# Optimization experiments

Measured on AMD Instinct MI355X. Metric: run time of the kernel, lower is better.

Reference implementation:

```python
import jax, jax.numpy as jnp
import numpy as np

PAD = 0

def setup_inputs() -> dict:
    key = jax.random.key(0)
    ks = jax.random.split(key, 16)
    B, S, D, F = 64, 512, 768, 256
    VOCAB = 32000
    # variable-length tweets: length in [8, S], rest is padding (token id PAD=0)
    lengths = jax.random.randint(ks[0], (B,), 8, S + 1)
    tok = jax.random.randint(ks[1], (B, S), 1, VOCAB)
    x = jnp.where(jnp.arange(S)[None, :] < lengths[:, None], tok, PAD)
    h = jax.random.normal(ks[2], (B, S, D), dtype=jnp.float32)
    sc = 0.02
    w2 = jax.random.normal(ks[3], (F, D, 2), dtype=jnp.float32) * sc
    b2 = jax.random.normal(ks[4], (F,), dtype=jnp.float32) * sc
    w3 = jax.random.normal(ks[5], (F, D, 3), dtype=jnp.float32) * sc
    b3 = jax.random.normal(ks[6], (F,), dtype=jnp.float32) * sc
    w4 = jax.random.normal(ks[7], (F, D, 4), dtype=jnp.float32) * sc
    b4 = jax.random.normal(ks[8], (F,), dtype=jnp.float32) * sc
    w5 = jax.random.normal(ks[9], (F, D, 5), dtype=jnp.float32) * sc
    b5 = jax.random.normal(ks[10], (F,), dtype=jnp.float32) * sc
    fc_w = jax.random.normal(ks[11], (1, 4 * F), dtype=jnp.float32) * sc
    fc_b = jax.random.normal(ks[12], (1,), dtype=jnp.float32) * sc
    return {"x": x, "h": h, "w2": w2, "b2": b2, "w3": w3, "b3": b3,
            "w4": w4, "b4": b4, "w5": w5, "b5": b5, "fc_w": fc_w, "fc_b": fc_b}


def _branch(hc, L, w, b):
    # hc: [B, D, S] front-compacted hidden states; w: [F, D, k]
    k = w.shape[-1]
    out = jax.lax.conv_general_dilated(
        hc, w, window_strides=(1,), padding='VALID',
        dimension_numbers=('NCH', 'OIH', 'NCH')) + b[None, :, None]  # [B,F,S-k+1]
    T = out.shape[-1]
    # conv position t is valid iff t + k - 1 < L  <=>  t < L - k + 1
    valid = jnp.arange(T)[None, :] < (L - k + 1)[:, None]           # [B,T]
    neg = jnp.asarray(-jnp.inf, out.dtype)
    pooled = jnp.max(jnp.where(valid[:, None, :], out, neg), axis=-1)  # [B,F]
    return jax.nn.relu(pooled)


def reference(x, h, w2, b2, w3, b3, w4, b4, w5, b5, fc_w, fc_b):
    mask = x != PAD                                   # [B,S]
    L = mask.sum(axis=1)                              # [B]
    # stable compaction: move non-pad token hidden states to the front, order preserved
    order = jnp.argsort(jnp.logical_not(mask), axis=1, stable=True)   # [B,S]
    hc = jnp.take_along_axis(h, order[..., None], axis=1)             # [B,S,D]
    hc = hc.transpose(0, 2, 1)                                        # [B,D,S]
    feats = jnp.concatenate([
        _branch(hc, L, w2, b2),
        _branch(hc, L, w3, b3),
        _branch(hc, L, w4, b4),
        _branch(hc, L, w5, b5),
    ], axis=-1)                                       # [B, 4F]
    logits = feats @ fc_w.T + fc_b                    # [B,1]
    return jax.nn.sigmoid(logits).squeeze(-1)         # [B]
```

## Files before the change

### kernel.cpp

```cpp
#include <hip/hip_runtime.h>
#include <stdint.h>

#define Bn 64
#define Sn 512
#define SPn 520
#define Dn 768
#define JSTRIDE 196608
#define ABUF 16640
#define BSLOT 8192
#define QS_A 28.222222f
#define SAQ 0.035433072f

typedef int iv4 __attribute__((ext_vector_type(4)));

static __device__ __forceinline__ signed char q8(float f, float s) {
  float t = __builtin_rintf(f * s);
  t = fmaxf(-127.f, fminf(127.f, t));
  return (signed char)(int)t;
}

static __device__ __forceinline__ void gload16(const void* g, void* l) {
  __builtin_amdgcn_global_load_lds(
      (const __attribute__((address_space(1))) unsigned int*)g,
      (__attribute__((address_space(3))) unsigned int*)l, 16, 0, 0);
}

template<int S, typename T, int N>
static __device__ __forceinline__ T (&sel(T (&a)[N], T (&b)[N]))[N] {
  if constexpr (S) return b; else return a;
}

__global__ __launch_bounds__(256) void stage_kernel(
    const int* __restrict__ x, const float* __restrict__ h,
    const float* __restrict__ w2, const float* __restrict__ w3,
    const float* __restrict__ w4, const float* __restrict__ w5,
    signed char* __restrict__ hcq, signed char* __restrict__ wq,
    float* __restrict__ fscale, int* __restrict__ Lout) {
  int tid = threadIdx.x, lane = tid & 63, wv = tid >> 6;
  if (blockIdx.x < 512) {
    int cidx = blockIdx.x;
    int b = cidx >> 3, rblk = cidx & 7;
    __shared__ unsigned long long masks[8];
    __shared__ short sidx[Sn];
    for (int c = wv; c < 8; c += 4) {
      unsigned long long m = __ballot(x[b * Sn + c * 64 + lane] != 0);
      if (lane == 0) masks[c] = m;
    }
    __syncthreads();
    int pref[9]; pref[0] = 0;
    #pragma unroll
    for (int c = 0; c < 8; ++c) pref[c + 1] = pref[c] + __popcll(masks[c]);
    int L = pref[8];
    if (rblk == 0 && tid == 0) Lout[b] = L;
    for (int p = tid; p < Sn; p += 256) {
      int c = p >> 6, l = p & 63;
      unsigned long long m = masks[c];
      if ((m >> l) & 1ull)
        sidx[pref[c] + __popcll(m & ((1ull << l) - 1ull))] = (short)p;
    }
    __syncthreads();
    int r0 = rblk * 65;
    for (int r = r0 + wv; r < r0 + 65; r += 4) {
      if (r < L) {
        signed char* dst = hcq + ((size_t)b * SPn + r) * Dn;
        const float* src = h + ((size_t)b * Sn + sidx[r]) * Dn;
        #pragma unroll
        for (int c = 0; c < 3; ++c) {
          int d = c * 256 + lane * 4;
          float4 v = *(const float4*)(src + d);
          char4 o = { q8(v.x, QS_A), q8(v.y, QS_A), q8(v.z, QS_A), q8(v.w, QS_A) };
          *(char4*)(dst + d) = o;
        }
      }
    }
  } else {
    __shared__ float sf[3840];
    __shared__ float smax[4];
    int bb = blockIdx.x - 512;
    int br = bb >> 8, f = bb & 255, k = br + 2;
    const float* w = (br == 0) ? w2 : (br == 1) ? w3 : (br == 2) ? w4 : w5;
    int mBase = 256 * ((br * (br + 3)) >> 1);
    const float* src = w + (size_t)f * Dn * k;
    int n = Dn * k;
    float mx = 0.f;
    for (int e = tid; e < n; e += 256) {
      float v = src[e];
      sf[e] = v;
      mx = fmaxf(mx, fabsf(v));
    }
    #pragma unroll
    for (int off = 32; off; off >>= 1) mx = fmaxf(mx, __shfl_xor(mx, off));
    if (lane == 0) smax[wv] = mx;
    __syncthreads();
    float M = fmaxf(fmaxf(smax[0], smax[1]), fmaxf(smax[2], smax[3]));
    M = fmaxf(M, 1e-30f);
    if (tid == 0) fscale[br * 256 + f] = M / 127.f;
    float qs = 127.f / M;
    for (int j = 0; j < k; ++j) {
      signed char* dst = wq + (size_t)(mBase + j * 256 + f) * Dn;
      for (int d4 = tid * 4; d4 < Dn; d4 += 1024) {
        char4 o = { q8(sf[(d4 + 0) * k + j], qs), q8(sf[(d4 + 1) * k + j], qs),
                    q8(sf[(d4 + 2) * k + j], qs), q8(sf[(d4 + 3) * k + j], qs) };
        *(char4*)(dst + d4) = o;
      }
    }
  }
}

__global__ __launch_bounds__(256) void fill_kernel(
    const int* __restrict__ Lbuf, int* __restrict__ plan,
    int* __restrict__ rowmap) {
  __shared__ int sOff[65];
  __shared__ int sL[64];
  int tid = threadIdx.x;
  if (tid < 64) {
    int L = Lbuf[tid];
    int SL = (L + 15) & ~15;
    int pre = SL;
    #pragma unroll
    for (int off = 1; off < 64; off <<= 1) {
      int y = __shfl_up(pre, off);
      if (tid >= off) pre += y;
    }
    sOff[tid] = pre - SL;
    sL[tid] = L;
    if (tid == 63) sOff[64] = pre;
  }
  __syncthreads();
  int b = blockIdx.x;
  int off = sOff[b], L = sL[b];
  int SL = (L + 15) & ~15;
  int enc = (b << 20) | (L << 10);
  for (int t = tid; t < SL; t += 256) rowmap[off + t] = enc | t;
  if (b == 0) {
    int M = sOff[64];
    if (tid == 0) plan[0] = (M + 255) >> 8;
    for (int p = M + tid; p < M + 264; p += 256)
      rowmap[p] = 512;
  }
}

template<int KK>
static __device__ __forceinline__ void stageAll(
    int d0, char* sA, char* sB, const char* const (&gA)[2], const char* gAt,
    const char* gB0, int lane, int wvoff) {
  int buf = d0 & 1;
  char* bB = sB + buf * (KK * BSLOT);
  int doff = d0 * 64;
  #pragma unroll
  for (int tap = 0; tap < KK; ++tap)
    gload16(gB0 + tap * JSTRIDE + doff, bB + tap * BSLOT + wvoff);
  char* nA = sA + buf * ABUF;
  gload16(gA[0] + doff, nA + wvoff);
  gload16(gA[1] + doff, nA + 8192 + wvoff);
  if (lane < 16) gload16(gAt + doff, nA + 16384);
}

static __device__ __forceinline__ void readFrag(
    int j, const char* curA, const char* bB, int wr, int wc, int lrow, int lg,
    iv4 (&Af)[4], iv4 (&Bf)[4]) {
  const char* curB = bB + j * BSLOT;
  #pragma unroll
  for (int n = 0; n < 4; ++n) {
    int row = wc * 64 + n * 16 + lrow;
    Bf[n] = *(const iv4*)(curB + row * 64 + ((lg ^ ((row >> 1) & 3)) << 4));
  }
  #pragma unroll
  for (int m = 0; m < 4; ++m) {
    int row = wr * 64 + m * 16 + lrow + j;
    Af[m] = *(const iv4*)(curA + row * 64 + ((lg ^ ((row >> 1) & 3)) << 4));
  }
}

template<int KK, int J>
static __device__ __forceinline__ void jpass(
    const char* curA, const char* bB, int wr, int wc, int lrow, int lg,
    iv4 (&Af0)[4], iv4 (&Bf0)[4], iv4 (&Af1)[4], iv4 (&Bf1)[4],
    iv4 (&acc)[4][4]) {
  if constexpr (J + 1 < KK)
    readFrag(J + 1, curA, bB, wr, wc, lrow, lg,
             sel<(J + 1) & 1>(Af0, Af1), sel<(J + 1) & 1>(Bf0, Bf1));
  iv4 (&Au)[4] = sel<J & 1>(Af0, Af1);
  iv4 (&Bu)[4] = sel<J & 1>(Bf0, Bf1);
  __builtin_amdgcn_s_setprio(1);
  #pragma unroll
  for (int n = 0; n < 4; ++n)
    #pragma unroll
    for (int m = 0; m < 4; ++m)
      acc[m][n] = __builtin_amdgcn_mfma_i32_16x16x64_i8(Au[m], Bu[n], acc[m][n], 0, 0, 0);
  __builtin_amdgcn_s_setprio(0);
}

template<int KK>
static __device__ __forceinline__ void computeD0(
    int d0, const char* sA, const char* sB, int wr, int wc, int lrow, int lg,
    iv4 (&acc)[4][4]) {
  int buf = d0 & 1;
  const char* curA = sA + buf * ABUF;
  const char* bB = sB + buf * (KK * BSLOT);
  iv4 Af0[4], Bf0[4], Af1[4], Bf1[4];
  readFrag(0, curA, bB, wr, wc, lrow, lg, Af0, Bf0);
  jpass<KK, 0>(curA, bB, wr, wc, lrow, lg, Af0, Bf0, Af1, Bf1, acc);
  if constexpr (KK > 1) jpass<KK, 1>(curA, bB, wr, wc, lrow, lg, Af0, Bf0, Af1, Bf1, acc);
  if constexpr (KK > 2) jpass<KK, 2>(curA, bB, wr, wc, lrow, lg, Af0, Bf0, Af1, Bf1, acc);
  if constexpr (KK > 3) jpass<KK, 3>(curA, bB, wr, wc, lrow, lg, Af0, Bf0, Af1, Bf1, acc);
  if constexpr (KK > 4) jpass<KK, 4>(curA, bB, wr, wc, lrow, lg, Af0, Bf0, Af1, Bf1, acc);
}

template<int KK>
static __device__ __forceinline__ void conv_loop(
    char* sA, char* sB, const char* const (&gA)[2], const char* gAt,
    const char* gB0, int lane, int wr, int wc, int lrow, int lg, int wvoff,
    iv4 (&acc)[4][4]) {
  stageAll<KK>(0, sA, sB, gA, gAt, gB0, lane, wvoff);
  __syncthreads();
  #pragma unroll 2
  for (int d0 = 0; d0 < 11; ++d0) {
    stageAll<KK>(d0 + 1, sA, sB, gA, gAt, gB0, lane, wvoff);
    computeD0<KK>(d0, sA, sB, wr, wc, lrow, lg, acc);
    __syncthreads();
  }
  computeD0<KK>(11, sA, sB, wr, wc, lrow, lg, acc);
}

__global__ __launch_bounds__(512) void conv_kernel(
    const signed char* __restrict__ hcq, const signed char* __restrict__ wq,
    const float* __restrict__ b2, const float* __restrict__ b3,
    const float* __restrict__ b4, const float* __restrict__ b5,
    const float* __restrict__ fscale,
    const int* __restrict__ plan, const int* __restrict__ rowmap,
    int* __restrict__ feats) {
  __shared__ char smem[2 * ABUF + 2 * 5 * BSLOT];
  char* sA = smem;
  char* sB = smem + 2 * ABUF;
  int idx = blockIdx.x;
  int xcd = idx & 7, s2 = idx >> 3;
  int sub = s2 & 7, tile = xcd + ((s2 >> 3) << 3);
  if (tile >= plan[0]) return;
  int br = 3 - (sub >> 1), ff = sub & 1, kk = br + 2;
  int mBase = 256 * ((br * (br + 3)) >> 1) + ff * 128;
  const float* bias = (br == 0) ? b2 : (br == 1) ? b3 : (br == 2) ? b4 : b5;
  int tid = threadIdx.x, lane = tid & 63, wv = tid >> 6;
  int wr = wv >> 1, wc = wv & 1;
  int lrow = lane & 15, lg = lane >> 4;
  int wvoff = wv * 1024;
  int P0 = tile << 8;

  const char* gA[2];
  #pragma unroll
  for (int p = 0; p < 2; ++p) {
    int c = p * 512 + tid;
    int row = c >> 2, sgp = c & 3;
    int rm = rowmap[P0 + row];
    int bb_ = rm >> 20, t = rm & 1023;
    int seg = sgp ^ ((row >> 1) & 3);
    gA[p] = (const char*)(hcq + ((size_t)(bb_ * SPn + t)) * Dn + seg * 16);
  }
  const char* gAt;
  {
    int l = lane & 15;
    int row = 256 + (l >> 2), sgp = l & 3;
    int rm = rowmap[P0 + row];
    int bb_ = rm >> 20, t = rm & 1023;
    int seg = sgp ^ ((row >> 1) & 3);
    gAt = (const char*)(hcq + ((size_t)(bb_ * SPn + t)) * Dn + seg * 16);
  }
  const char* gB0;
  {
    int row = tid >> 2, sgp = tid & 3;
    int seg = sgp ^ ((row >> 1) & 3);
    gB0 = (const char*)(wq + ((size_t)(mBase + row)) * Dn + seg * 16);
  }

  iv4 acc[4][4];
  #pragma unroll
  for (int m = 0; m < 4; ++m)
    #pragma unroll
    for (int n = 0; n < 4; ++n) acc[m][n] = (iv4)0;

  switch (br) {
    case 3: conv_loop<5>(sA, sB, gA, gAt, gB0, lane, wr, wc, lrow, lg, wvoff, acc); break;
    case 2: conv_loop<4>(sA, sB, gA, gAt, gB0, lane, wr, wc, lrow, lg, wvoff, acc); break;
    case 1: conv_loop<3>(sA, sB, gA, gAt, gB0, lane, wr, wc, lrow, lg, wvoff, acc); break;
    default: conv_loop<2>(sA, sB, gA, gAt, gB0, lane, wr, wc, lrow, lg, wvoff, acc); break;
  }

  int rmv[4];
  #pragma unroll
  for (int m = 0; m < 4; ++m) rmv[m] = rowmap[P0 + wr * 64 + m * 16];
  #pragma unroll
  for (int n = 0; n < 4; ++n) {
    int fg = ff * 128 + wc * 64 + n * 16 + lrow;
    float bv = bias[fg];
    float sfc = fscale[br * 256 + fg] * SAQ;
    #pragma unroll
    for (int m = 0; m < 4; ++m) {
      int bb_ = rmv[m] >> 20;
      int Lb = (rmv[m] >> 10) & 1023;
      int t0 = (rmv[m] & 1023) + lg * 4;
      int vlim = Lb - kk + 1;
      float pmax = 0.f;
      #pragma unroll
      for (int i = 0; i < 4; ++i) {
        float v = (float)acc[m][n][i] * sfc + bv;
        pmax = fmaxf(pmax, (t0 + i < vlim) ? fmaxf(v, 0.f) : 0.f);
      }
      pmax = fmaxf(pmax, __shfl_xor(pmax, 16));
      pmax = fmaxf(pmax, __shfl_xor(pmax, 32));
      if (lane < 16 && pmax > 0.f)
        atomicMax(feats + bb_ * 1024 + br * 256 + fg, __float_as_int(pmax));
    }
  }
}

__global__ __launch_bounds__(64) void fc_kernel(
    const int* __restrict__ feats, const float* __restrict__ fcw,
    const float* __restrict__ fcb, float* __restrict__ out) {
  int b = blockIdx.x, lane = threadIdx.x;
  float acc = 0.f;
  for (int i = lane; i < 1024; i += 64)
    acc += __int_as_float(feats[b * 1024 + i]) * fcw[i];
  #pragma unroll
  for (int off = 32; off; off >>= 1) acc += __shfl_xor(acc, off);
  if (lane == 0) out[b] = 1.f / (1.f + expf(-(acc + fcb[0])));
}

extern "C" void kernel_launch(void* const* d_in, const int* in_sizes, int n_in,
                              void* d_out, int out_size, void* d_ws, size_t ws_size,
                              hipStream_t stream) {
  const int*   x   = (const int*)d_in[0];
  const float* h   = (const float*)d_in[1];
  const float* w2  = (const float*)d_in[2];
  const float* b2  = (const float*)d_in[3];
  const float* w3  = (const float*)d_in[4];
  const float* b3  = (const float*)d_in[5];
  const float* w4  = (const float*)d_in[6];
  const float* b4  = (const float*)d_in[7];
  const float* w5  = (const float*)d_in[8];
  const float* b5  = (const float*)d_in[9];
  const float* fcw = (const float*)d_in[10];
  const float* fcb = (const float*)d_in[11];
  float* out = (float*)d_out;
  char* ws = (char*)d_ws;
  signed char* hcq = (signed char*)ws;
  signed char* wq  = (signed char*)(ws + 25559040);
  float* fscale = (float*)(ws + 28311552);
  int* feats  = (int*)(ws + 28315648);
  int* Lbuf   = (int*)(ws + 28577792);
  int* plan   = (int*)(ws + 28578048);
  int* rowmap = (int*)(ws + 28578064);

  hipMemsetAsync(feats, 0, 64 * 1024 * 4, stream);
  stage_kernel<<<1536, 256, 0, stream>>>(x, h, w2, w3, w4, w5, hcq, wq, fscale, Lbuf);
  fill_kernel<<<64, 256, 0, stream>>>(Lbuf, plan, rowmap);
  conv_kernel<<<1024, 512, 0, stream>>>(hcq, wq, b2, b3, b4, b5, fscale, plan, rowmap, feats);
  fc_kernel<<<64, 64, 0, stream>>>(feats, fcw, fcb, out);
}
```

Baseline: 98.00 us.

## Single-buffer weight tiles in LDS and raise occupancy target of conv kernel

Weight (B) tiles change from double-buffered to single-buffered in LDS, which shrinks shared memory per block. Input (A) tiles stay double-buffered and are prefetched one step ahead. Weight loads now sit behind an extra barrier after compute, and launch bounds ask for 4 blocks per CU, so more blocks fit per CU at the cost of serialising weight loads with compute. The register double-buffered fragment prefetch across taps is dropped for a simpler per-tap load-then-MFMA loop, which cuts register pressure but exposes LDS read latency.

```diff
diff --git a/kernel.cpp b/kernel.cpp
--- a/kernel.cpp
+++ b/kernel.cpp
@@ -23,11 +23,6 @@
   __builtin_amdgcn_global_load_lds(
       (const __attribute__((address_space(1))) unsigned int*)g,
       (__attribute__((address_space(3))) unsigned int*)l, 16, 0, 0);
-}
-
-template<int S, typename T, int N>
-static __device__ __forceinline__ T (&sel(T (&a)[N], T (&b)[N]))[N] {
-  if constexpr (S) return b; else return a;
 }
 
 __global__ __launch_bounds__(256) void stage_kernel(
@@ -140,71 +135,52 @@
   }
 }
 
+static __device__ __forceinline__ void issueA(
+    int d0i, char* sA, const char* const (&gA)[2], const char* gAt,
+    int lane, int wvoff) {
+  int aoff = (d0i + 1) * 64;
+  char* nA = sA + ((d0i + 1) & 1) * ABUF;
+  gload16(gA[0] + aoff, nA + wvoff);
+  gload16(gA[1] + aoff, nA + 8192 + wvoff);
+  if (lane < 16) gload16(gAt + aoff, nA + 16384);
+}
+
 template<int KK>
-static __device__ __forceinline__ void stageAll(
-    int d0, char* sA, char* sB, const char* const (&gA)[2], const char* gAt,
-    const char* gB0, int lane, int wvoff) {
-  int buf = d0 & 1;
-  char* bB = sB + buf * (KK * BSLOT);
+static __device__ __forceinline__ void stageB(
+    int d0, char* sB, const char* gB0, int wvoff) {
   int doff = d0 * 64;
   #pragma unroll
   for (int tap = 0; tap < KK; ++tap)
-    gload16(gB0 + tap * JSTRIDE + doff, bB + tap * BSLOT + wvoff);
-  char* nA = sA + buf * ABUF;
-  gload16(gA[0] + doff, nA + wvoff);
-  gload16(gA[1] + doff, nA + 8192 + wvoff);
-  if (lane < 16) gload16(gAt + doff, nA + 16384);
-}
-
-static __device__ __forceinline__ void readFrag(
-    int j, const char* curA, const char* bB, int wr, int wc, int lrow, int lg,
-    iv4 (&Af)[4], iv4 (&Bf)[4]) {
-  const char* curB = bB + j * BSLOT;
-  #pragma unroll
-  for (int n = 0; n < 4; ++n) {
-    int row = wc * 64 + n * 16 + lrow;
-    Bf[n] = *(const iv4*)(curB + row * 64 + ((lg ^ ((row >> 1) & 3)) << 4));
-  }
-  #pragma unroll
-  for (int m = 0; m < 4; ++m) {
-    int row = wr * 64 + m * 16 + lrow + j;
-    Af[m] = *(const iv4*)(curA + row * 64 + ((lg ^ ((row >> 1) & 3)) << 4));
-  }
-}
-
-template<int KK, int J>
-static __device__ __forceinline__ void jpass(
-    const char* curA, const char* bB, int wr, int wc, int lrow, int lg,
-    iv4 (&Af0)[4], iv4 (&Bf0)[4], iv4 (&Af1)[4], iv4 (&Bf1)[4],
-    iv4 (&acc)[4][4]) {
-  if constexpr (J + 1 < KK)
-    readFrag(J + 1, curA, bB, wr, wc, lrow, lg,
-             sel<(J + 1) & 1>(Af0, Af1), sel<(J + 1) & 1>(Bf0, Bf1));
-  iv4 (&Au)[4] = sel<J & 1>(Af0, Af1);
-  iv4 (&Bu)[4] = sel<J & 1>(Bf0, Bf1);
-  __builtin_amdgcn_s_setprio(1);
-  #pragma unroll
-  for (int n = 0; n < 4; ++n)
-    #pragma unroll
-    for (int m = 0; m < 4; ++m)
-      acc[m][n] = __builtin_amdgcn_mfma_i32_16x16x64_i8(Au[m], Bu[n], acc[m][n], 0, 0, 0);
-  __builtin_amdgcn_s_setprio(0);
+    gload16(gB0 + tap * JSTRIDE + doff, sB + tap * BSLOT + wvoff);
 }
 
 template<int KK>
 static __device__ __forceinline__ void computeD0(
     int d0, const char* sA, const char* sB, int wr, int wc, int lrow, int lg,
     iv4 (&acc)[4][4]) {
-  int buf = d0 & 1;
-  const char* curA = sA + buf * ABUF;
-  const char* bB = sB + buf * (KK * BSLOT);
-  iv4 Af0[4], Bf0[4], Af1[4], Bf1[4];
-  readFrag(0, curA, bB, wr, wc, lrow, lg, Af0, Bf0);
-  jpass<KK, 0>(curA, bB, wr, wc, lrow, lg, Af0, Bf0, Af1, Bf1, acc);
-  if constexpr (KK > 1) jpass<KK, 1>(curA, bB, wr, wc, lrow, lg, Af0, Bf0, Af1, Bf1, acc);
-  if constexpr (KK > 2) jpass<KK, 2>(curA, bB, wr, wc, lrow, lg, Af0, Bf0, Af1, Bf1, acc);
-  if constexpr (KK > 3) jpass<KK, 3>(curA, bB, wr, wc, lrow, lg, Af0, Bf0, Af1, Bf1, acc);
-  if constexpr (KK > 4) jpass<KK, 4>(curA, bB, wr, wc, lrow, lg, Af0, Bf0, Af1, Bf1, acc);
+  const char* curA = sA + (d0 & 1) * ABUF;
+  #pragma unroll
+  for (int j = 0; j < KK; ++j) {
+    const char* curB = sB + j * BSLOT;
+    iv4 Af[4], Bf[4];
+    #pragma unroll
+    for (int n = 0; n < 4; ++n) {
+      int row = wc * 64 + n * 16 + lrow;
+      Bf[n] = *(const iv4*)(curB + row * 64 + ((lg ^ ((row >> 1) & 3)) << 4));
+    }
+    #pragma unroll
+    for (int m = 0; m < 4; ++m) {
+      int row = wr * 64 + m * 16 + lrow + j;
+      Af[m] = *(const iv4*)(curA + row * 64 + ((lg ^ ((row >> 1) & 3)) << 4));
+    }
+    __builtin_amdgcn_s_setprio(1);
+    #pragma unroll
+    for (int n = 0; n < 4; ++n)
+      #pragma unroll
+      for (int m = 0; m < 4; ++m)
+        acc[m][n] = __builtin_amdgcn_mfma_i32_16x16x64_i8(Af[m], Bf[n], acc[m][n], 0, 0, 0);
+    __builtin_amdgcn_s_setprio(0);
+  }
 }
 
 template<int KK>
@@ -212,25 +188,30 @@
     char* sA, char* sB, const char* const (&gA)[2], const char* gAt,
     const char* gB0, int lane, int wr, int wc, int lrow, int lg, int wvoff,
     iv4 (&acc)[4][4]) {
-  stageAll<KK>(0, sA, sB, gA, gAt, gB0, lane, wvoff);
+  gload16(gA[0], sA + wvoff);
+  gload16(gA[1], sA + 8192 + wvoff);
+  if (lane < 16) gload16(gAt, sA + 16384);
+  stageB<KK>(0, sB, gB0, wvoff);
   __syncthreads();
-  #pragma unroll 2
-  for (int d0 = 0; d0 < 11; ++d0) {
-    stageAll<KK>(d0 + 1, sA, sB, gA, gAt, gB0, lane, wvoff);
+  for (int d0 = 0; d0 < 12; ++d0) {
+    if (d0 < 11) issueA(d0, sA, gA, gAt, lane, wvoff);
     computeD0<KK>(d0, sA, sB, wr, wc, lrow, lg, acc);
     __syncthreads();
-  }
-  computeD0<KK>(11, sA, sB, wr, wc, lrow, lg, acc);
-}
-
-__global__ __launch_bounds__(512) void conv_kernel(
+    if (d0 < 11) {
+      stageB<KK>(d0 + 1, sB, gB0, wvoff);
+      __syncthreads();
+    }
+  }
+}
+
+__global__ __launch_bounds__(512, 4) void conv_kernel(
     const signed char* __restrict__ hcq, const signed char* __restrict__ wq,
     const float* __restrict__ b2, const float* __restrict__ b3,
     const float* __restrict__ b4, const float* __restrict__ b5,
     const float* __restrict__ fscale,
     const int* __restrict__ plan, const int* __restrict__ rowmap,
     int* __restrict__ feats) {
-  __shared__ char smem[2 * ABUF + 2 * 5 * BSLOT];
+  __shared__ char smem[2 * ABUF + 5 * BSLOT];
   char* sA = smem;
   char* sB = smem + 2 * ABUF;
   int idx = blockIdx.x;
```

Result: slower. 106.7 us (+8.9%).
